# Optimization experiments

Measured on AMD Instinct MI355X. Metric: run time of the kernel, lower is better.

The kernel has to match this reference:

```python
import jax, jax.numpy as jnp
import numpy as np

T, S, C = 256, 2048, 128
HID = 32      # MLP hidden (hardcoded in module)
G = 64        # gru_input_size
L = 64        # latent_size (GRU hidden)


def setup_inputs() -> dict:
    key = jax.random.key(0)
    ks = jax.random.split(key, 9)
    sc = lambda fan_in: 1.0 / np.sqrt(fan_in)
    return {
        "x": jax.random.normal(ks[0], (T, S, C), dtype=jnp.float32),
        # MLP: C -> 32 -> G, LeakyReLU after each layer
        "W1": jax.random.normal(ks[1], (C, HID), dtype=jnp.float32) * sc(C),
        "b1": jnp.zeros((HID,), jnp.float32),
        "W2": jax.random.normal(ks[2], (HID, G), dtype=jnp.float32) * sc(HID),
        "b2": jnp.zeros((G,), jnp.float32),
        # GRU params, PyTorch layout: W_ih (3L, G), W_hh (3L, L), gates ordered [r, z, n]
        "W_ih": jax.random.normal(ks[3], (3 * L, G), dtype=jnp.float32) * sc(L),
        "W_hh": jax.random.normal(ks[4], (3 * L, L), dtype=jnp.float32) * sc(L),
        "b_ih": jax.random.normal(ks[5], (3 * L,), dtype=jnp.float32) * sc(L),
        "b_hh": jax.random.normal(ks[6], (3 * L,), dtype=jnp.float32) * sc(L),
    }


def _lrelu(v):
    return jnp.where(v >= 0, v, 0.01 * v)


def reference(x, W1, b1, W2, b2, W_ih, W_hh, b_ih, b_hh):
    # Batched MLP projection over all (t, stock) pairs: (T,S,C) -> (T,S,G)
    h_proj = _lrelu(_lrelu(x @ W1 + b1) @ W2 + b2)

    # Precompute input-side gate activations for all timesteps: (T,S,3L)
    gx_all = h_proj @ W_ih.T + b_ih

    def step(h, gx):
        gh = h @ W_hh.T + b_hh  # (S, 3L)
        r = jax.nn.sigmoid(gx[:, :L] + gh[:, :L])
        z = jax.nn.sigmoid(gx[:, L:2 * L] + gh[:, L:2 * L])
        n = jnp.tanh(gx[:, 2 * L:] + r * gh[:, 2 * L:])
        h_new = (1.0 - z) * n + z * h
        return h_new, None

    h0 = jnp.zeros((S, L), jnp.float32)
    hT, _ = jax.lax.scan(step, h0, gx_all)
    return hT  # (stock_size, latent_size)
```

## Files before the change

### kernel.cpp

```cpp
#include <hip/hip_runtime.h>
#include <hip/hip_bf16.h>

#define T_TOT 256
#define S_TOT 2048
#define C_IN  128
#define HID_  32
#define G_    64
#define L_    64

typedef __attribute__((ext_vector_type(8))) short short8;
typedef __attribute__((ext_vector_type(4))) float f32x4;

#define MFMA(a, b, c) __builtin_amdgcn_mfma_f32_16x16x32_bf16((a), (b), (c), 0, 0, 0)

__device__ __forceinline__ void fsplit(float v, ushort& hi, ushort& lo) {
    __hip_bfloat16 h = __float2bfloat16(v);
    float hf = __bfloat162float(h);
    __hip_bfloat16 l = __float2bfloat16(v - hf);
    hi = *reinterpret_cast<ushort*>(&h);
    lo = *reinterpret_cast<ushort*>(&l);
}

__device__ __forceinline__ float lrelu(float v) { return v >= 0.f ? v : 0.01f * v; }

__device__ __forceinline__ float sig1(float x) {
    x = fminf(fmaxf(x, -30.f), 30.f);
    return __builtin_amdgcn_rcpf(1.f + __expf(-x));
}
__device__ __forceinline__ float th1(float x) {
    x = fminf(fmaxf(x, -15.f), 15.f);
    float e = __expf(-2.f * x);
    return (1.f - e) * __builtin_amdgcn_rcpf(1.f + e);
}

__global__ __launch_bounds__(256, 2)
void mlp_kernel(const float* __restrict__ x,
                const float* __restrict__ W1, const float* __restrict__ b1,
                const float* __restrict__ W2, const float* __restrict__ b2,
                float* __restrict__ hpws)
{
    __shared__ ushort w1h[32][128], w1l[32][128];
    __shared__ ushort w2h[64][32],  w2l[64][32];
    __shared__ ushort xh[4][16][128], xl[4][16][128];
    __shared__ ushort h1h[4][16][32], h1l[4][16][32];

    const int tid = threadIdx.x;
    const int w = tid >> 6, l = tid & 63;
    const int lg = l >> 4, lr = l & 15;

#pragma unroll
    for (int i = 0; i < 16; ++i) {
        int e = tid + 256 * i;
        int k = e >> 5, n = e & 31;
        ushort hi, lo; fsplit(W1[e], hi, lo);
        int by = (2 * k) ^ ((n & 7) << 4);
        *(ushort*)((char*)&w1h[n][0] + by) = hi;
        *(ushort*)((char*)&w1l[n][0] + by) = lo;
    }
#pragma unroll
    for (int i = 0; i < 8; ++i) {
        int e = tid + 256 * i;
        int k = e >> 6, n = e & 63;
        ushort hi, lo; fsplit(W2[e], hi, lo);
        int by = (2 * k) ^ ((n & 3) << 4);
        *(ushort*)((char*)&w2h[n][0] + by) = hi;
        *(ushort*)((char*)&w2l[n][0] + by) = lo;
    }

    const size_t row0 = (size_t)blockIdx.x * 64 + w * 16;
    const float4* xg = (const float4*)(x + row0 * C_IN);
#pragma unroll
    for (int i = 0; i < 8; ++i) {
        int f4 = l + 64 * i;
        int r = f4 >> 5, c4 = f4 & 31;
        float4 v = xg[f4];
        ushort h4[4], l4[4];
        fsplit(v.x, h4[0], l4[0]);
        fsplit(v.y, h4[1], l4[1]);
        fsplit(v.z, h4[2], l4[2]);
        fsplit(v.w, h4[3], l4[3]);
        int by = (8 * c4) ^ ((r & 7) << 4);
        ushort4 ph = {h4[0], h4[1], h4[2], h4[3]};
        ushort4 pl = {l4[0], l4[1], l4[2], l4[3]};
        *(ushort4*)((char*)&xh[w][r][0] + by) = ph;
        *(ushort4*)((char*)&xl[w][r][0] + by) = pl;
    }
    __syncthreads();

    f32x4 h1acc[2];
#pragma unroll
    for (int nt = 0; nt < 2; ++nt) {
        int col = lr + 16 * nt;
        float bb = b1[col];
        f32x4 acc = {bb, bb, bb, bb};
#pragma unroll
        for (int ks = 0; ks < 4; ++ks) {
            int aby = (64 * ks + 16 * lg) ^ ((lr & 7) << 4);
            short8 ahi = *(short8*)((char*)&xh[w][lr][0] + aby);
            short8 alo = *(short8*)((char*)&xl[w][lr][0] + aby);
            int bby = (64 * ks + 16 * lg) ^ ((col & 7) << 4);
            short8 bhi = *(short8*)((char*)&w1h[col][0] + bby);
            short8 blo = *(short8*)((char*)&w1l[col][0] + bby);
            acc = MFMA(ahi, bhi, acc);
            acc = MFMA(ahi, blo, acc);
            acc = MFMA(alo, bhi, acc);
        }
        h1acc[nt] = acc;
    }
#pragma unroll
    for (int nt = 0; nt < 2; ++nt) {
        int col = lr + 16 * nt;
#pragma unroll
        for (int r = 0; r < 4; ++r) {
            float v = lrelu(h1acc[nt][r]);
            ushort hi, lo; fsplit(v, hi, lo);
            int row = 4 * lg + r;
            int by = (2 * col) ^ ((row & 3) << 4);
            *(ushort*)((char*)&h1h[w][row][0] + by) = hi;
            *(ushort*)((char*)&h1l[w][row][0] + by) = lo;
        }
    }
    __syncthreads();

    f32x4 hpacc[4];
#pragma unroll
    for (int nt = 0; nt < 4; ++nt) {
        int col = lr + 16 * nt;
        float bb = b2[col];
        f32x4 acc = {bb, bb, bb, bb};
        int aby = (16 * lg) ^ ((lr & 3) << 4);
        short8 ahi = *(short8*)((char*)&h1h[w][lr][0] + aby);
        short8 alo = *(short8*)((char*)&h1l[w][lr][0] + aby);
        int bby = (16 * lg) ^ ((col & 3) << 4);
        short8 bhi = *(short8*)((char*)&w2h[col][0] + bby);
        short8 blo = *(short8*)((char*)&w2l[col][0] + bby);
        acc = MFMA(ahi, bhi, acc);
        acc = MFMA(ahi, blo, acc);
        acc = MFMA(alo, bhi, acc);
        hpacc[nt] = acc;
    }
    __syncthreads();
#pragma unroll
    for (int nt = 0; nt < 4; ++nt) {
        int col = lr + 16 * nt;
#pragma unroll
        for (int r = 0; r < 4; ++r) {
            float v = lrelu(hpacc[nt][r]);
            ushort hi, lo; fsplit(v, hi, lo);
            int row = 4 * lg + r;
            int by = (2 * col) ^ ((row & 7) << 4);
            *(ushort*)((char*)&xh[w][row][0] + by) = hi;
            *(ushort*)((char*)&xl[w][row][0] + by) = lo;
        }
    }
    __syncthreads();

    const size_t rt = row0 >> 4;
    float4* outw = (float4*)hpws;
#pragma unroll
    for (int ks = 0; ks < 2; ++ks) {
        int by = (64 * ks + 16 * lg) ^ ((lr & 7) << 4);
        short8 fh = *(short8*)((char*)&xh[w][lr][0] + by);
        short8 fl = *(short8*)((char*)&xl[w][lr][0] + by);
        outw[((rt * 2 + ks) * 2 + 0) * 64 + l] = *(float4*)&fh;
        outw[((rt * 2 + ks) * 2 + 1) * 64 + l] = *(float4*)&fl;
    }
}

__device__ __forceinline__ void gstep(
    const short8 (&cur)[2][2], short8 (&pf)[2][2], int t,
    const short8* __restrict__ hpg, int b, int l, int lg, int lr, int colr,
    const short8 (&wih_h)[3][2], const short8 (&wih_l)[3][2],
    const short8 (&whh_h)[3][2], const short8 (&whh_l)[3][2],
    const float (&bih)[3], const float (&bhh)[3],
    f32x4& hprev, int& p, ushort* hbh, ushort* hbl)
{
    if (t + 2 < T_TOT) {
        size_t rt = (size_t)(t + 2) * 128 + b;
#pragma unroll
        for (int ks = 0; ks < 2; ++ks)
#pragma unroll
            for (int pl = 0; pl < 2; ++pl)
                pf[ks][pl] = hpg[((rt * 2 + ks) * 2 + pl) * 64 + l];
    }

    const ushort* rh = hbh + p * 1024;
    const ushort* rl = hbl + p * 1024;
    short8 ah[2], al[2];
#pragma unroll
    for (int ks = 0; ks < 2; ++ks) {
        int by = (64 * ks + 16 * lg) ^ ((lr & 7) << 4);
        ah[ks] = *(short8*)((char*)(rh + lr * 64) + by);
        al[ks] = *(short8*)((char*)(rl + lr * 64) + by);
    }

    f32x4 agx[3], agh[3];
#pragma unroll
    for (int g = 0; g < 3; ++g) {
        f32x4 c0 = {bih[g], bih[g], bih[g], bih[g]};
        f32x4 c1 = {0.f, 0.f, 0.f, 0.f};
        f32x4 c2 = {0.f, 0.f, 0.f, 0.f};
        c0 = MFMA(cur[0][0], wih_h[g][0], c0);
        c1 = MFMA(cur[0][0], wih_l[g][0], c1);
        c2 = MFMA(cur[0][1], wih_h[g][0], c2);
        c0 = MFMA(cur[1][0], wih_h[g][1], c0);
        c1 = MFMA(cur[1][0], wih_l[g][1], c1);
        c2 = MFMA(cur[1][1], wih_h[g][1], c2);
        agx[g] = c0 + c1 + c2;
    }
#pragma unroll
    for (int g = 0; g < 3; ++g) {
        f32x4 c0 = {bhh[g], bhh[g], bhh[g], bhh[g]};
        f32x4 c1 = {0.f, 0.f, 0.f, 0.f};
        f32x4 c2 = {0.f, 0.f, 0.f, 0.f};
        c0 = MFMA(ah[0], whh_h[g][0], c0);
        c1 = MFMA(ah[0], whh_l[g][0], c1);
        c2 = MFMA(al[0], whh_h[g][0], c2);
        c0 = MFMA(ah[1], whh_h[g][1], c0);
        c1 = MFMA(ah[1], whh_l[g][1], c1);
        c2 = MFMA(al[1], whh_h[g][1], c2);
        agh[g] = c0 + c1 + c2;
    }

    f32x4 hn;
#pragma unroll
    for (int r = 0; r < 4; ++r) {
        float rr = sig1(agx[0][r] + agh[0][r]);
        float zz = sig1(agx[1][r] + agh[1][r]);
        float nn = th1(agx[2][r] + rr * agh[2][r]);
        hn[r] = (1.f - zz) * nn + zz * hprev[r];
    }

    ushort* wh = hbh + (p ^ 1) * 1024;
    ushort* wl = hbl + (p ^ 1) * 1024;
#pragma unroll
    for (int r = 0; r < 4; ++r) {
        ushort hi, lo; fsplit(hn[r], hi, lo);
        int row = 4 * lg + r;
        int by = (2 * colr) ^ ((row & 7) << 4);
        *(ushort*)((char*)(wh + row * 64) + by) = hi;
        *(ushort*)((char*)(wl + row * 64) + by) = lo;
    }
    hprev = hn;

    asm volatile("s_waitcnt lgkmcnt(0)\n\ts_barrier" ::: "memory");
    p ^= 1;
}

__global__ __launch_bounds__(256, 1)
void gru_kernel(const float* __restrict__ hpws_f,
                const float* __restrict__ W_ih, const float* __restrict__ W_hh,
                const float* __restrict__ b_ih, const float* __restrict__ b_hh,
                float* __restrict__ out)
{
    __shared__ ushort hbh_s[2][16][64], hbl_s[2][16][64];

    const int tid = threadIdx.x;
    const int w = tid >> 6, l = tid & 63;
    const int lg = l >> 4, lr = l & 15;
    const int colr = 16 * w + lr;
    const int b = blockIdx.x;
    ushort* hbh = &hbh_s[0][0][0];
    ushort* hbl = &hbl_s[0][0][0];

    short8 wih_h[3][2], wih_l[3][2], whh_h[3][2], whh_l[3][2];
    float bih[3], bhh[3];
#pragma unroll
    for (int g = 0; g < 3; ++g) {
        int n = colr + 64 * g;
        bih[g] = b_ih[n];
        bhh[g] = b_hh[n];
#pragma unroll
        for (int ks = 0; ks < 2; ++ks) {
            const float* pp = W_ih + n * 64 + 32 * ks + 8 * lg;
            const float* qq = W_hh + n * 64 + 32 * ks + 8 * lg;
            short8 ph, pl, qh, ql;
#pragma unroll
            for (int j = 0; j < 8; ++j) {
                ushort hi, lo;
                fsplit(pp[j], hi, lo); ph[j] = (short)hi; pl[j] = (short)lo;
                fsplit(qq[j], hi, lo); qh[j] = (short)hi; ql[j] = (short)lo;
            }
            wih_h[g][ks] = ph; wih_l[g][ks] = pl;
            whh_h[g][ks] = qh; whh_l[g][ks] = ql;
        }
    }

    f32x4 hprev = {0.f, 0.f, 0.f, 0.f};
#pragma unroll
    for (int r = 0; r < 4; ++r) {
        int row = 4 * lg + r;
        int by = (2 * colr) ^ ((row & 7) << 4);
        *(ushort*)((char*)(hbh + row * 64) + by) = 0;
        *(ushort*)((char*)(hbl + row * 64) + by) = 0;
    }
    asm volatile("s_waitcnt lgkmcnt(0)\n\ts_barrier" ::: "memory");
    int p = 0;

    const short8* hpg = (const short8*)hpws_f;
    short8 ring[3][2][2];
#pragma unroll
    for (int tt = 0; tt < 2; ++tt) {
        size_t rt = (size_t)tt * 128 + b;
#pragma unroll
        for (int ks = 0; ks < 2; ++ks)
#pragma unroll
            for (int pl = 0; pl < 2; ++pl)
                ring[tt][ks][pl] = hpg[((rt * 2 + ks) * 2 + pl) * 64 + l];
    }

    for (int tb = 0; tb < 255; tb += 3) {
        gstep(ring[0], ring[2], tb + 0, hpg, b, l, lg, lr, colr,
              wih_h, wih_l, whh_h, whh_l, bih, bhh, hprev, p, hbh, hbl);
        gstep(ring[1], ring[0], tb + 1, hpg, b, l, lg, lr, colr,
              wih_h, wih_l, whh_h, whh_l, bih, bhh, hprev, p, hbh, hbl);
        gstep(ring[2], ring[1], tb + 2, hpg, b, l, lg, lr, colr,
              wih_h, wih_l, whh_h, whh_l, bih, bhh, hprev, p, hbh, hbl);
    }
    gstep(ring[0], ring[2], 255, hpg, b, l, lg, lr, colr,
          wih_h, wih_l, whh_h, whh_l, bih, bhh, hprev, p, hbh, hbl);

#pragma unroll
    for (int r = 0; r < 4; ++r)
        out[(16 * b + 4 * lg + r) * 64 + colr] = hprev[r];
}

extern "C" void kernel_launch(void* const* d_in, const int* in_sizes, int n_in,
                              void* d_out, int out_size, void* d_ws, size_t ws_size,
                              hipStream_t stream)
{
    const float* x    = (const float*)d_in[0];
    const float* W1   = (const float*)d_in[1];
    const float* b1   = (const float*)d_in[2];
    const float* W2   = (const float*)d_in[3];
    const float* b2   = (const float*)d_in[4];
    const float* W_ih = (const float*)d_in[5];
    const float* W_hh = (const float*)d_in[6];
    const float* b_ih = (const float*)d_in[7];
    const float* b_hh = (const float*)d_in[8];
    float* out  = (float*)d_out;
    float* hpws = (float*)d_ws;

    mlp_kernel<<<(T_TOT * S_TOT) / 64, 256, 0, stream>>>(x, W1, b1, W2, b2, hpws);
    gru_kernel<<<S_TOT / 16, 256, 0, stream>>>(hpws, W_ih, W_hh, b_ih, b_hh, out);
}
```

Baseline: 606.1 us.

## Pre-split MLP weights once, load x straight to registers, pipeline GRU input gates

Result: no change. 595.3 us (-1.8%).

```diff
diff --git a/kernel.cpp b/kernel.cpp
--- a/kernel.cpp
+++ b/kernel.cpp
@@ -33,168 +33,152 @@
     return (1.f - e) * __builtin_amdgcn_rcpf(1.f + e);
 }
 
-__global__ __launch_bounds__(256, 2)
+__global__ void wsetup_kernel(const float* __restrict__ W1,
+                              const float* __restrict__ W2,
+                              float4* __restrict__ w1f, float4* __restrict__ w2f)
+{
+    const int tid = threadIdx.x;
+#pragma unroll
+    for (int i = 0; i < 4; ++i) {
+        int e = tid + 256 * i;
+        int l = e & 63, idx = e >> 6;
+        int pl = idx & 1, ks = (idx >> 1) & 3, nt = idx >> 3;
+        int lg = l >> 4, lr = l & 15;
+        short8 v;
+#pragma unroll
+        for (int j = 0; j < 8; ++j) {
+            ushort hi, lo;
+            fsplit(W1[(32 * ks + 8 * lg + j) * HID_ + (lr + 16 * nt)], hi, lo);
+            v[j] = (short)(pl ? lo : hi);
+        }
+        w1f[e] = *(float4*)&v;
+    }
+#pragma unroll
+    for (int i = 0; i < 2; ++i) {
+        int e = tid + 256 * i;
+        int l = e & 63, idx = e >> 6;
+        int pl = idx & 1, nt = idx >> 1;
+        int lg = l >> 4, lr = l & 15;
+        short8 v;
+#pragma unroll
+        for (int j = 0; j < 8; ++j) {
+            ushort hi, lo;
+            fsplit(W2[(8 * lg + j) * G_ + (lr + 16 * nt)], hi, lo);
+            v[j] = (short)(pl ? lo : hi);
+        }
+        w2f[e] = *(float4*)&v;
+    }
+}
+
+__global__ __launch_bounds__(256, 3)
 void mlp_kernel(const float* __restrict__ x,
-                const float* __restrict__ W1, const float* __restrict__ b1,
-                const float* __restrict__ W2, const float* __restrict__ b2,
+                const float* __restrict__ b1, const float* __restrict__ b2,
+                const float4* __restrict__ w1f, const float4* __restrict__ w2f,
                 float* __restrict__ hpws)
 {
-    __shared__ ushort w1h[32][128], w1l[32][128];
-    __shared__ ushort w2h[64][32],  w2l[64][32];
-    __shared__ ushort xh[4][16][128], xl[4][16][128];
-    __shared__ ushort h1h[4][16][32], h1l[4][16][32];
+    __shared__ ushort h1b[4][2][16][32];
+    __shared__ ushort hpb[4][2][16][64];
 
     const int tid = threadIdx.x;
     const int w = tid >> 6, l = tid & 63;
     const int lg = l >> 4, lr = l & 15;
-
-#pragma unroll
-    for (int i = 0; i < 16; ++i) {
-        int e = tid + 256 * i;
-        int k = e >> 5, n = e & 31;
-        ushort hi, lo; fsplit(W1[e], hi, lo);
-        int by = (2 * k) ^ ((n & 7) << 4);
-        *(ushort*)((char*)&w1h[n][0] + by) = hi;
-        *(ushort*)((char*)&w1l[n][0] + by) = lo;
-    }
-#pragma unroll
-    for (int i = 0; i < 8; ++i) {
-        int e = tid + 256 * i;
-        int k = e >> 6, n = e & 63;
-        ushort hi, lo; fsplit(W2[e], hi, lo);
-        int by = (2 * k) ^ ((n & 3) << 4);
-        *(ushort*)((char*)&w2h[n][0] + by) = hi;
-        *(ushort*)((char*)&w2l[n][0] + by) = lo;
-    }
-
     const size_t row0 = (size_t)blockIdx.x * 64 + w * 16;
-    const float4* xg = (const float4*)(x + row0 * C_IN);
-#pragma unroll
-    for (int i = 0; i < 8; ++i) {
-        int f4 = l + 64 * i;
-        int r = f4 >> 5, c4 = f4 & 31;
-        float4 v = xg[f4];
-        ushort h4[4], l4[4];
-        fsplit(v.x, h4[0], l4[0]);
-        fsplit(v.y, h4[1], l4[1]);
-        fsplit(v.z, h4[2], l4[2]);
-        fsplit(v.w, h4[3], l4[3]);
-        int by = (8 * c4) ^ ((r & 7) << 4);
-        ushort4 ph = {h4[0], h4[1], h4[2], h4[3]};
-        ushort4 pl = {l4[0], l4[1], l4[2], l4[3]};
-        *(ushort4*)((char*)&xh[w][r][0] + by) = ph;
-        *(ushort4*)((char*)&xl[w][r][0] + by) = pl;
-    }
-    __syncthreads();
+
+    short8 ahi[4], alo[4];
+    const float* xr = x + (row0 + lr) * C_IN + 8 * lg;
+#pragma unroll
+    for (int ks = 0; ks < 4; ++ks) {
+        float4 u0 = *(const float4*)(xr + 32 * ks);
+        float4 u1 = *(const float4*)(xr + 32 * ks + 4);
+        ushort hi, lo;
+        fsplit(u0.x, hi, lo); ahi[ks][0] = (short)hi; alo[ks][0] = (short)lo;
+        fsplit(u0.y, hi, lo); ahi[ks][1] = (short)hi; alo[ks][1] = (short)lo;
+        fsplit(u0.z, hi, lo); ahi[ks][2] = (short)hi; alo[ks][2] = (short)lo;
+        fsplit(u0.w, hi, lo); ahi[ks][3] = (short)hi; alo[ks][3] = (short)lo;
+        fsplit(u1.x, hi, lo); ahi[ks][4] = (short)hi; alo[ks][4] = (short)lo;
+        fsplit(u1.y, hi, lo); ahi[ks][5] = (short)hi; alo[ks][5] = (short)lo;
+        fsplit(u1.z, hi, lo); ahi[ks][6] = (short)hi; alo[ks][6] = (short)lo;
+        fsplit(u1.w, hi, lo); ahi[ks][7] = (short)hi; alo[ks][7] = (short)lo;
+    }
 
     f32x4 h1acc[2];
 #pragma unroll
     for (int nt = 0; nt < 2; ++nt) {
-        int col = lr + 16 * nt;
-        float bb = b1[col];
+        float bb = b1[lr + 16 * nt];
         f32x4 acc = {bb, bb, bb, bb};
 #pragma unroll
         for (int ks = 0; ks < 4; ++ks) {
-            int aby = (64 * ks + 16 * lg) ^ ((lr & 7) << 4);
-            short8 ahi = *(short8*)((char*)&xh[w][lr][0] + aby);
-            short8 alo = *(short8*)((char*)&xl[w][lr][0] + aby);
-            int bby = (64 * ks + 16 * lg) ^ ((col & 7) << 4);
-            short8 bhi = *(short8*)((char*)&w1h[col][0] + bby);
-            short8 blo = *(short8*)((char*)&w1l[col][0] + bby);
-            acc = MFMA(ahi, bhi, acc);
-            acc = MFMA(ahi, blo, acc);
-            acc = MFMA(alo, bhi, acc);
+            short8 bhi = *(const short8*)&w1f[((nt * 4 + ks) * 2 + 0) * 64 + l];
+            short8 blo = *(const short8*)&w1f[((nt * 4 + ks) * 2 + 1) * 64 + l];
+            acc = MFMA(ahi[ks], bhi, acc);
+            acc = MFMA(ahi[ks], blo, acc);
+            acc = MFMA(alo[ks], bhi, acc);
         }
         h1acc[nt] = acc;
     }
 #pragma unroll
     for (int nt = 0; nt < 2; ++nt) {
-        int col = lr + 16 * nt;
 #pragma unroll
         for (int r = 0; r < 4; ++r) {
             float v = lrelu(h1acc[nt][r]);
             ushort hi, lo; fsplit(v, hi, lo);
-            int row = 4 * lg + r;
+            int row = 4 * lg + r, col = lr + 16 * nt;
             int by = (2 * col) ^ ((row & 3) << 4);
-            *(ushort*)((char*)&h1h[w][row][0] + by) = hi;
-            *(ushort*)((char*)&h1l[w][row][0] + by) = lo;
-        }
-    }
-    __syncthreads();
+            *(ushort*)((char*)&h1b[w][0][row][0] + by) = hi;
+            *(ushort*)((char*)&h1b[w][1][row][0] + by) = lo;
+        }
+    }
+    asm volatile("s_waitcnt lgkmcnt(0)" ::: "memory");
+    short8 a1h, a1l;
+    {
+        int aby = (16 * lg) ^ ((lr & 3) << 4);
+        a1h = *(short8*)((char*)&h1b[w][0][lr][0] + aby);
+        a1l = *(short8*)((char*)&h1b[w][1][lr][0] + aby);
+    }
 
     f32x4 hpacc[4];
 #pragma unroll
     for (int nt = 0; nt < 4; ++nt) {
-        int col = lr + 16 * nt;
-        float bb = b2[col];
+        float bb = b2[lr + 16 * nt];
         f32x4 acc = {bb, bb, bb, bb};
-        int aby = (16 * lg) ^ ((lr & 3) << 4);
-        short8 ahi = *(short8*)((char*)&h1h[w][lr][0] + aby);
-        short8 alo = *(short8*)((char*)&h1l[w][lr][0] + aby);
-        int bby = (16 * lg) ^ ((col & 3) << 4);
-        short8 bhi = *(short8*)((char*)&w2h[col][0] + bby);
-        short8 blo = *(short8*)((char*)&w2l[col][0] + bby);
-        acc = MFMA(ahi, bhi, acc);
-        acc = MFMA(ahi, blo, acc);
-        acc = MFMA(alo, bhi, acc);
+        short8 bhi = *(const short8*)&w2f[(nt * 2 + 0) * 64 + l];
+        short8 blo = *(const short8*)&w2f[(nt * 2 + 1) * 64 + l];
+        acc = MFMA(a1h, bhi, acc);
+        acc = MFMA(a1h, blo, acc);
+        acc = MFMA(a1l, bhi, acc);
         hpacc[nt] = acc;
     }
-    __syncthreads();
 #pragma unroll
     for (int nt = 0; nt < 4; ++nt) {
-        int col = lr + 16 * nt;
 #pragma unroll
         for (int r = 0; r < 4; ++r) {
             float v = lrelu(hpacc[nt][r]);
             ushort hi, lo; fsplit(v, hi, lo);
-            int row = 4 * lg + r;
+            int row = 4 * lg + r, col = lr + 16 * nt;
             int by = (2 * col) ^ ((row & 7) << 4);
-            *(ushort*)((char*)&xh[w][row][0] + by) = hi;
-            *(ushort*)((char*)&xl[w][row][0] + by) = lo;
-        }
-    }
-    __syncthreads();
+            *(ushort*)((char*)&hpb[w][0][row][0] + by) = hi;
+            *(ushort*)((char*)&hpb[w][1][row][0] + by) = lo;
+        }
+    }
+    asm volatile("s_waitcnt lgkmcnt(0)" ::: "memory");
 
     const size_t rt = row0 >> 4;
     float4* outw = (float4*)hpws;
 #pragma unroll
     for (int ks = 0; ks < 2; ++ks) {
         int by = (64 * ks + 16 * lg) ^ ((lr & 7) << 4);
-        short8 fh = *(short8*)((char*)&xh[w][lr][0] + by);
-        short8 fl = *(short8*)((char*)&xl[w][lr][0] + by);
+        short8 fh = *(short8*)((char*)&hpb[w][0][lr][0] + by);
+        short8 fl = *(short8*)((char*)&hpb[w][1][lr][0] + by);
         outw[((rt * 2 + ks) * 2 + 0) * 64 + l] = *(float4*)&fh;
         outw[((rt * 2 + ks) * 2 + 1) * 64 + l] = *(float4*)&fl;
     }
 }
 
-__device__ __forceinline__ void gstep(
-    const short8 (&cur)[2][2], short8 (&pf)[2][2], int t,
-    const short8* __restrict__ hpg, int b, int l, int lg, int lr, int colr,
+__device__ __forceinline__ void gxcalc(
+    const short8 (&cur)[2][2],
     const short8 (&wih_h)[3][2], const short8 (&wih_l)[3][2],
-    const short8 (&whh_h)[3][2], const short8 (&whh_l)[3][2],
-    const float (&bih)[3], const float (&bhh)[3],
-    f32x4& hprev, int& p, ushort* hbh, ushort* hbl)
-{
-    if (t + 2 < T_TOT) {
-        size_t rt = (size_t)(t + 2) * 128 + b;
-#pragma unroll
-        for (int ks = 0; ks < 2; ++ks)
-#pragma unroll
-            for (int pl = 0; pl < 2; ++pl)
-                pf[ks][pl] = hpg[((rt * 2 + ks) * 2 + pl) * 64 + l];
-    }
-
-    const ushort* rh = hbh + p * 1024;
-    const ushort* rl = hbl + p * 1024;
-    short8 ah[2], al[2];
-#pragma unroll
-    for (int ks = 0; ks < 2; ++ks) {
-        int by = (64 * ks + 16 * lg) ^ ((lr & 7) << 4);
-        ah[ks] = *(short8*)((char*)(rh + lr * 64) + by);
-        al[ks] = *(short8*)((char*)(rl + lr * 64) + by);
-    }
-
-    f32x4 agx[3], agh[3];
+    const float (&bih)[3], f32x4 (&agx)[3])
+{
 #pragma unroll
     for (int g = 0; g < 3; ++g) {
         f32x4 c0 = {bih[g], bih[g], bih[g], bih[g]};
@@ -208,6 +192,40 @@
         c2 = MFMA(cur[1][1], wih_h[g][1], c2);
         agx[g] = c0 + c1 + c2;
     }
+}
+
+__device__ __forceinline__ void gstep(
+    const f32x4 (&gxin)[3], f32x4 (&gxout)[3],
+    const short8 (&nring)[2][2], short8 (&pf)[2][2], int t, bool last,
+    const short8* __restrict__ hpg, int b, int l, int lg, int lr, int colr,
+    const short8 (&wih_h)[3][2], const short8 (&wih_l)[3][2],
+    const short8 (&whh_h)[3][2], const short8 (&whh_l)[3][2],
+    const float (&bih)[3], const float (&bhh)[3],
+    f32x4& hprev, int& p, ushort* hbh, ushort* hbl)
+{
+    if (t + 2 < T_TOT) {
+        size_t rtn = (size_t)(t + 2) * 128 + b;
+#pragma unroll
+        for (int ks = 0; ks < 2; ++ks)
+#pragma unroll
+            for (int pl = 0; pl < 2; ++pl)
+                pf[ks][pl] = hpg[((rtn * 2 + ks) * 2 + pl) * 64 + l];
+    }
+
+    const ushort* rh = hbh + p * 1024;
+    const ushort* rl = hbl + p * 1024;
+    short8 ah[2], al[2];
+#pragma unroll
+    for (int ks = 0; ks < 2; ++ks) {
+        int by = (64 * ks + 16 * lg) ^ ((lr & 7) << 4);
+        ah[ks] = *(short8*)((char*)(rh + lr * 64) + by);
+        al[ks] = *(short8*)((char*)(rl + lr * 64) + by);
+    }
+
+    if (!last)
+        gxcalc(nring, wih_h, wih_l, bih, gxout);
+
+    f32x4 agh[3];
 #pragma unroll
     for (int g = 0; g < 3; ++g) {
         f32x4 c0 = {bhh[g], bhh[g], bhh[g], bhh[g]};
@@ -225,10 +243,10 @@
     f32x4 hn;
 #pragma unroll
     for (int r = 0; r < 4; ++r) {
-        float rr = sig1(agx[0][r] + agh[0][r]);
-        float zz = sig1(agx[1][r] + agh[1][r]);
-        float nn = th1(agx[2][r] + rr * agh[2][r]);
-        hn[r] = (1.f - zz) * nn + zz * hprev[r];
+        float rr = sig1(gxin[0][r] + agh[0][r]);
+        float zz = sig1(gxin[1][r] + agh[1][r]);
+        float nn = th1(gxin[2][r] + rr * agh[2][r]);
+        hn[r] = fmaf(zz, hprev[r] - nn, nn);
     }
 
     ushort* wh = hbh + (p ^ 1) * 1024;
@@ -298,7 +316,7 @@
     int p = 0;
 
     const short8* hpg = (const short8*)hpws_f;
-    short8 ring[3][2][2];
+    short8 ring[4][2][2];
 #pragma unroll
     for (int tt = 0; tt < 2; ++tt) {
         size_t rt = (size_t)tt * 128 + b;
@@ -309,15 +327,26 @@
                 ring[tt][ks][pl] = hpg[((rt * 2 + ks) * 2 + pl) * 64 + l];
     }
 
-    for (int tb = 0; tb < 255; tb += 3) {
-        gstep(ring[0], ring[2], tb + 0, hpg, b, l, lg, lr, colr,
+    f32x4 gxA[3], gxB[3];
+    gxcalc(ring[0], wih_h, wih_l, bih, gxA);
+
+    for (int tb = 0; tb < 252; tb += 4) {
+        gstep(gxA, gxB, ring[1], ring[2], tb + 0, false, hpg, b, l, lg, lr, colr,
               wih_h, wih_l, whh_h, whh_l, bih, bhh, hprev, p, hbh, hbl);
-        gstep(ring[1], ring[0], tb + 1, hpg, b, l, lg, lr, colr,
+        gstep(gxB, gxA, ring[2], ring[3], tb + 1, false, hpg, b, l, lg, lr, colr,
               wih_h, wih_l, whh_h, whh_l, bih, bhh, hprev, p, hbh, hbl);
-        gstep(ring[2], ring[1], tb + 2, hpg, b, l, lg, lr, colr,
+        gstep(gxA, gxB, ring[3], ring[0], tb + 2, false, hpg, b, l, lg, lr, colr,
               wih_h, wih_l, whh_h, whh_l, bih, bhh, hprev, p, hbh, hbl);
-    }
-    gstep(ring[0], ring[2], 255, hpg, b, l, lg, lr, colr,
+        gstep(gxB, gxA, ring[0], ring[1], tb + 3, false, hpg, b, l, lg, lr, colr,
+              wih_h, wih_l, whh_h, whh_l, bih, bhh, hprev, p, hbh, hbl);
+    }
+    gstep(gxA, gxB, ring[1], ring[2], 252, false, hpg, b, l, lg, lr, colr,
+          wih_h, wih_l, whh_h, whh_l, bih, bhh, hprev, p, hbh, hbl);
+    gstep(gxB, gxA, ring[2], ring[3], 253, false, hpg, b, l, lg, lr, colr,
+          wih_h, wih_l, whh_h, whh_l, bih, bhh, hprev, p, hbh, hbl);
+    gstep(gxA, gxB, ring[3], ring[0], 254, false, hpg, b, l, lg, lr, colr,
+          wih_h, wih_l, whh_h, whh_l, bih, bhh, hprev, p, hbh, hbl);
+    gstep(gxB, gxA, ring[0], ring[1], 255, true, hpg, b, l, lg, lr, colr,
           wih_h, wih_l, whh_h, whh_l, bih, bhh, hprev, p, hbh, hbl);
 
 #pragma unroll
@@ -338,9 +367,13 @@
     const float* W_hh = (const float*)d_in[6];
     const float* b_ih = (const float*)d_in[7];
     const float* b_hh = (const float*)d_in[8];
-    float* out  = (float*)d_out;
-    float* hpws = (float*)d_ws;
-
-    mlp_kernel<<<(T_TOT * S_TOT) / 64, 256, 0, stream>>>(x, W1, b1, W2, b2, hpws);
-    gru_kernel<<<S_TOT / 16, 256, 0, stream>>>(hpws, W_ih, W_hh, b_ih, b_hh, out);
-}
+    float* out = (float*)d_out;
+
+    float4* w1f = (float4*)d_ws;
+    float4* w2f = w1f + 1024;
+    float*  hp  = (float*)((char*)d_ws + 32 * 1024);
+
+    wsetup_kernel<<<1, 256, 0, stream>>>(W1, W2, w1f, w2f);
+    mlp_kernel<<<(T_TOT * S_TOT) / 64, 256, 0, stream>>>(x, b1, b2, w1f, w2f, hp);
+    gru_kernel<<<S_TOT / 16, 256, 0, stream>>>(hp, W_ih, W_hh, b_ih, b_hh, out);
+}
```
